# Kernel optimization log

Hardware: AMD Instinct MI355X
Metric: run time of the kernel (lower is better)

Reference implementation:

```python
import jax, jax.numpy as jnp
import numpy as np

N = 100000      # nodes
E = 1600000     # edges (before self loops)
IN_F = 128
OUT_F = 32
HEADS = 4
NEG_SLOPE = 0.2


def setup_inputs() -> dict:
    key = jax.random.key(0)
    k1, k2, k3, k4, k5, k6 = jax.random.split(key, 6)
    x = jax.random.normal(k1, (N, IN_F), dtype=jnp.float32)
    edge_index = jax.random.randint(k2, (2, E), 0, N, dtype=jnp.int64)
    # PyG GATConv params: shared linear W [in, H*F], attention vectors att_src/att_dst [1,H,F], bias [H*F]
    glorot = (6.0 / (IN_F + HEADS * OUT_F)) ** 0.5
    W = jax.random.uniform(k3, (IN_F, HEADS * OUT_F), dtype=jnp.float32, minval=-glorot, maxval=glorot)
    ga = (6.0 / (1 + OUT_F)) ** 0.5
    att_src = jax.random.uniform(k4, (HEADS, OUT_F), dtype=jnp.float32, minval=-ga, maxval=ga)
    att_dst = jax.random.uniform(k5, (HEADS, OUT_F), dtype=jnp.float32, minval=-ga, maxval=ga)
    bias = jnp.zeros((HEADS * OUT_F,), dtype=jnp.float32)
    return {"x": x, "edge_index": edge_index, "W": W, "att_src": att_src, "att_dst": att_dst, "bias": bias}


def reference(x, edge_index, W, att_src, att_dst, bias):
    n = x.shape[0]
    # add self loops (PyG add_self_loops=True)
    loops = jnp.arange(n, dtype=edge_index.dtype)
    src = jnp.concatenate([edge_index[0], loops])  # [E+N] message source j
    dst = jnp.concatenate([edge_index[1], loops])  # [E+N] message target i

    h = (x @ W).reshape(n, HEADS, OUT_F)                 # [N,H,F]
    a_src = jnp.sum(h * att_src[None], axis=-1)          # [N,H]
    a_dst = jnp.sum(h * att_dst[None], axis=-1)          # [N,H]

    e = a_src[src] + a_dst[dst]                          # [E',H]
    e = jax.nn.leaky_relu(e, NEG_SLOPE)
    # per-destination softmax over incoming edges
    m = jax.ops.segment_max(e, dst, num_segments=n)      # [N,H]
    ex = jnp.exp(e - m[dst])
    s = jax.ops.segment_sum(ex, dst, num_segments=n)     # [N,H]
    alpha = ex / (s[dst] + 1e-16)                        # [E',H]

    msg = h[src] * alpha[:, :, None]                     # [E',H,F]
    out = jax.ops.segment_sum(msg, dst, num_segments=n)  # [N,H,F]
    return out.reshape(n, HEADS * OUT_F) + bias
```

## Files before the change

kernel.cpp:

```cpp
#include <hip/hip_runtime.h>


#define NEG_SLOPE 0.2f
#define NB_MAX 256
#define BSHIFT 9
#define CHUNK 4096
#define BCAP 12288
#define CAP 11264
#define SS_STRIDE 11520
#define LOG2E 1.4426950408889634f

typedef __attribute__((ext_vector_type(8))) short short8;
typedef __attribute__((ext_vector_type(4))) float f32x4;
typedef __attribute__((ext_vector_type(2))) float f32x2;

__device__ __forceinline__ unsigned int rne16(unsigned int u) {
  return (u + 0x7fffu + ((u >> 16) & 1u)) >> 16;
}
__device__ __forceinline__ unsigned int f2bf_pack(float a, float b) {
  return (rne16(__float_as_uint(b)) << 16) | (rne16(__float_as_uint(a)) & 0xffffu);
}

__global__ __launch_bounds__(256) void k_prep(
    const float* __restrict__ W, unsigned short* __restrict__ Wt,
    int* __restrict__ bcnt) {
  int tid = threadIdx.x;
  if (blockIdx.x == 64) { bcnt[tid] = 0; return; }
  int idx = blockIdx.x * 256 + tid;
  int k = idx >> 7, col = idx & 127;
  Wt[col * 128 + k] = (unsigned short)rne16(__float_as_uint(W[idx]));
}

__global__ __launch_bounds__(256) void k_binmm(
    const int* __restrict__ ei, int* __restrict__ bcnt,
    unsigned int* __restrict__ binned, int E, int Nn, int nb, int nbBin,
    const float* __restrict__ x, const unsigned short* __restrict__ Wt,
    unsigned int* __restrict__ hb,
    const float* __restrict__ attS, const float* __restrict__ attD,
    float* __restrict__ aS, float* __restrict__ aD) {
  __shared__ unsigned int buf[CHUNK];
  __shared__ unsigned char bkt[CHUNK];
  __shared__ int hist[NB_MAX];
  __shared__ int loc[NB_MAX];
  __shared__ int gbase[NB_MAX];
  int tid = threadIdx.x;

  if ((int)blockIdx.x < nbBin) {
    int e0 = blockIdx.x * CHUNK;
    int n = E - e0; if (n > CHUNK) n = CHUNK;

    hist[tid] = 0;
    __syncthreads();

    int dstv[CHUNK / 256];
    int srcv[CHUNK / 256];
    int rankv[CHUNK / 256];
#pragma unroll
    for (int j = 0; j < CHUNK / 256; ++j) {
      int idx = j * 256 + tid;
      dstv[j] = -1;
      if (idx < n) {
        int d = ei[E + e0 + idx];
        srcv[j] = ei[e0 + idx];
        dstv[j] = d;
        rankv[j] = atomicAdd(&hist[d >> BSHIFT], 1);
      }
    }
    __syncthreads();

    if (tid < 64) {
      int base = tid * 4;
      int v0 = hist[base], v1 = hist[base + 1], v2 = hist[base + 2], v3 = hist[base + 3];
      int s = v0 + v1 + v2 + v3;
      int inc = s;
#pragma unroll
      for (int d = 1; d < 64; d <<= 1) {
        int t = __shfl_up(inc, d, 64);
        if (tid >= d) inc += t;
      }
      int ex = inc - s;
      loc[base] = ex; loc[base + 1] = ex + v0;
      loc[base + 2] = ex + v0 + v1; loc[base + 3] = ex + v0 + v1 + v2;
    }
    __syncthreads();

#pragma unroll
    for (int j = 0; j < CHUNK / 256; ++j) {
      if (dstv[j] >= 0) {
        int b = dstv[j] >> BSHIFT;
        int slot = loc[b] + rankv[j];
        buf[slot] = (unsigned)srcv[j] | ((unsigned)(dstv[j] & 511) << 20);
        bkt[slot] = (unsigned char)b;
      }
    }
    for (int b = tid; b < nb; b += 256)
      if (hist[b] > 0) gbase[b] = atomicAdd(&bcnt[b], hist[b]);
    __syncthreads();

    for (int s = tid; s < n; s += 256) {
      int b = bkt[s];
      binned[(unsigned)b * BCAP + gbase[b] + (s - loc[b])] = buf[s];
    }
    return;
  }

  int gbid = blockIdx.x - nbBin;
  int w = tid >> 6, lane = tid & 63;
  int m = lane & 15, q = lane >> 4;
  int r0 = gbid * 64 + w * 16;
  int rowA = r0 + m; if (rowA >= Nn) rowA = Nn - 1;
  const float* xrow = x + (unsigned)rowA * 128u;

  f32x4 acc[8];
#pragma unroll
  for (int t = 0; t < 8; ++t) acc[t] = (f32x4){0.f, 0.f, 0.f, 0.f};

#pragma unroll
  for (int ks = 0; ks < 4; ++ks) {
    int k0 = ks * 32 + q * 8;
    float4 a0 = *(const float4*)(xrow + k0);
    float4 a1 = *(const float4*)(xrow + k0 + 4);
    unsigned au[4];
    au[0] = f2bf_pack(a0.x, a0.y);
    au[1] = f2bf_pack(a0.z, a0.w);
    au[2] = f2bf_pack(a1.x, a1.y);
    au[3] = f2bf_pack(a1.z, a1.w);
    short8 af = *(short8*)au;
#pragma unroll
    for (int t = 0; t < 8; ++t) {
      short8 bf = *(const short8*)(Wt + (unsigned)(t * 16 + m) * 128u + k0);
      acc[t] = __builtin_amdgcn_mfma_f32_16x16x32_bf16(af, bf, acc[t], 0, 0, 0);
    }
  }

  float sSa[4], sSb[4], sDa[4], sDb[4];
#pragma unroll
  for (int u = 0; u < 4; ++u) {
    sSa[u] = attS[u * 32 + m]; sSb[u] = attS[u * 32 + m + 16];
    sDa[u] = attD[u * 32 + m]; sDb[u] = attD[u * 32 + m + 16];
  }

#pragma unroll
  for (int r = 0; r < 4; ++r) {
    int rowo = r0 + q * 4 + r;
    bool ok = rowo < Nn;
    if (ok) {
#pragma unroll
      for (int u = 0; u < 4; ++u)
        hb[(unsigned)rowo * 64u + u * 16 + m] = f2bf_pack(acc[2 * u][r], acc[2 * u + 1][r]);
    }
#pragma unroll
    for (int u = 0; u < 4; ++u) {
      float pS = acc[2 * u][r] * sSa[u] + acc[2 * u + 1][r] * sSb[u];
      float pD = acc[2 * u][r] * sDa[u] + acc[2 * u + 1][r] * sDb[u];
#pragma unroll
      for (int d = 8; d >= 1; d >>= 1) {
        pS += __shfl_down(pS, d, 16);
        pD += __shfl_down(pD, d, 16);
      }
      if (ok && m == 0) {
        aS[(unsigned)rowo * 4u + u] = pS * LOG2E;
        aD[(unsigned)rowo * 4u + u] = pD * LOG2E;
      }
    }
  }
}

__global__ __launch_bounds__(512) void k_scatter2(
    const unsigned int* __restrict__ binned, const int* __restrict__ bcnt,
    int2* __restrict__ off2, int* __restrict__ ssrc, int Nn) {
  __shared__ int cnt[512];
  __shared__ int obuf[CAP];
  __shared__ int wsum[8];
  int b = blockIdx.x, tid = threadIdx.x;
  int node0 = b << BSHIFT;
  int nnodes = Nn - node0; if (nnodes > 512) nnodes = 512;
  int nE = bcnt[b];
  const unsigned* bp = binned + (unsigned)b * BCAP;

  cnt[tid] = 0;
  __syncthreads();
  for (int i = tid; i < nE; i += 512)
    atomicAdd(&cnt[(bp[i] >> 20) & 511u], 1);
  __syncthreads();

  int v = cnt[tid] + (tid < nnodes ? 1 : 0);
  int lane = tid & 63, w = tid >> 6;
  int inc = v;
#pragma unroll
  for (int d = 1; d < 64; d <<= 1) {
    int t = __shfl_up(inc, d, 64);
    if (lane >= d) inc += t;
  }
  if (lane == 63) wsum[w] = inc;
  __syncthreads();
  int wbase = 0;
  for (int ww = 0; ww < w; ++ww) wbase += wsum[ww];
  int ex = wbase + inc - v;
  __syncthreads();

  int csrBase = b * SS_STRIDE;
  if (tid < nnodes) {
    off2[node0 + tid] = make_int2(csrBase + ex, v);
    obuf[ex] = node0 + tid;
  }
  cnt[tid] = ex + 1;
  __syncthreads();

  for (int i = tid; i < nE; i += 512) {
    unsigned p = bp[i];
    int d = (p >> 20) & 511u;
    int pos = atomicAdd(&cnt[d], 1);
    if (pos < CAP) obuf[pos] = (int)(p & 0xFFFFFu);
  }
  __syncthreads();

  int tot = nE + nnodes;
  for (int i = tid; i < tot; i += 512) ssrc[csrBase + i] = obuf[i];
}

__global__ __launch_bounds__(256) void k_aggregate(
    const unsigned int* __restrict__ hb, const float* __restrict__ aS, const float* __restrict__ aD,
    const int2* __restrict__ off2, const int* __restrict__ ssrc,
    const float* __restrict__ bias, float* __restrict__ out, int Nn) {
  int wave = threadIdx.x >> 6;
  int lane = threadIdx.x & 63;
  int node = blockIdx.x * 4 + wave;
  if (node >= Nn) return;
  int un = __builtin_amdgcn_readfirstlane(node);
  unsigned hd = (unsigned)lane >> 4;
  float ad = aD[(unsigned)un * 4u + hd];
  int2 o = off2[un];
  int p0 = o.x;
  int deg = o.y;
  const int* sp = ssrc + p0;
  int nch = deg >> 2;
  f32x2 acc = {0.f, 0.f};
  float denA = 0.f, denB = 0.f;

  int s0 = 0, s1 = 0, s2 = 0, s3 = 0;
  unsigned v0 = 0, v1 = 0, v2 = 0, v3 = 0;
  float a0 = 0.f, a1 = 0.f, a2 = 0.f, a3 = 0.f;
  if (nch > 0) {
    s0 = sp[0]; s1 = sp[1]; s2 = sp[2]; s3 = sp[3];
    v0 = hb[(unsigned)s0 * 64u + lane]; v1 = hb[(unsigned)s1 * 64u + lane];
    v2 = hb[(unsigned)s2 * 64u + lane]; v3 = hb[(unsigned)s3 * 64u + lane];
    a0 = aS[(unsigned)s0 * 4u + hd]; a1 = aS[(unsigned)s1 * 4u + hd];
    a2 = aS[(unsigned)s2 * 4u + hd]; a3 = aS[(unsigned)s3 * 4u + hd];
    sp += 4;
  }
  for (int c = 0; c < nch; ++c) {
    int t0 = 0, t1 = 0, t2 = 0, t3 = 0;
    unsigned w0 = 0, w1 = 0, w2 = 0, w3 = 0;
    float b0 = 0.f, b1 = 0.f, b2 = 0.f, b3 = 0.f;
    if (c + 1 < nch) {
      t0 = sp[0]; t1 = sp[1]; t2 = sp[2]; t3 = sp[3];
      w0 = hb[(unsigned)t0 * 64u + lane]; w1 = hb[(unsigned)t1 * 64u + lane];
      w2 = hb[(unsigned)t2 * 64u + lane]; w3 = hb[(unsigned)t3 * 64u + lane];
      b0 = aS[(unsigned)t0 * 4u + hd]; b1 = aS[(unsigned)t1 * 4u + hd];
      b2 = aS[(unsigned)t2 * 4u + hd]; b3 = aS[(unsigned)t3 * 4u + hd];
      sp += 4;
    }
    float e0 = a0 + ad, e1 = a1 + ad, e2 = a2 + ad, e3 = a3 + ad;
    e0 = fmaxf(e0, NEG_SLOPE * e0); e1 = fmaxf(e1, NEG_SLOPE * e1);
    e2 = fmaxf(e2, NEG_SLOPE * e2); e3 = fmaxf(e3, NEG_SLOPE * e3);
    float x0 = exp2f(e0), x1 = exp2f(e1), x2 = exp2f(e2), x3 = exp2f(e3);
    denA += x0 + x1; denB += x2 + x3;
    f32x2 h0 = { __uint_as_float(v0 << 16), __uint_as_float(v0 & 0xffff0000u) };
    f32x2 h1 = { __uint_as_float(v1 << 16), __uint_as_float(v1 & 0xffff0000u) };
    f32x2 h2 = { __uint_as_float(v2 << 16), __uint_as_float(v2 & 0xffff0000u) };
    f32x2 h3 = { __uint_as_float(v3 << 16), __uint_as_float(v3 & 0xffff0000u) };
    acc = h0 * x0 + acc;
    acc = h1 * x1 + acc;
    acc = h2 * x2 + acc;
    acc = h3 * x3 + acc;
    s0 = t0; s1 = t1; s2 = t2; s3 = t3;
    v0 = w0; v1 = w1; v2 = w2; v3 = w3;
    a0 = b0; a1 = b1; a2 = b2; a3 = b3;
  }
  for (int p = nch << 2; p < deg; ++p) {
    int src = (ssrc + p0)[p];
    float e = aS[(unsigned)src * 4u + hd] + ad;
    e = fmaxf(e, NEG_SLOPE * e);
    float ex = exp2f(e);
    unsigned v = hb[(unsigned)src * 64u + lane];
    f32x2 hh = { __uint_as_float(v << 16), __uint_as_float(v & 0xffff0000u) };
    acc = hh * ex + acc;
    denA += ex;
  }
  float inv = 1.0f / (denA + denB + 1e-16f);
  unsigned col = hd * 32u + ((unsigned)lane & 15u);
  out[(unsigned)un * 128u + col] = acc.x * inv + bias[col];
  out[(unsigned)un * 128u + col + 16u] = acc.y * inv + bias[col + 16];
}

extern "C" void kernel_launch(void* const* d_in, const int* in_sizes, int n_in,
                              void* d_out, int out_size, void* d_ws, size_t ws_size,
                              hipStream_t stream) {
  const float* x    = (const float*)d_in[0];
  const int*   ei   = (const int*)d_in[1];
  const float* W    = (const float*)d_in[2];
  const float* attS = (const float*)d_in[3];
  const float* attD = (const float*)d_in[4];
  const float* bias = (const float*)d_in[5];
  float* out = (float*)d_out;

  const int Nn = in_sizes[0] / 128;
  const int E  = in_sizes[1] / 2;
  const int nb = (Nn + (1 << BSHIFT) - 1) >> BSHIFT;
  const int nbBin = (E + CHUNK - 1) / CHUNK;
  const int nGemm = (Nn + 63) / 64;

  char* ws = (char*)d_ws;
  size_t o = 0;
  auto take = [&](size_t bytes) { void* p = ws + o; o += (bytes + 255) & ~(size_t)255; return p; };
  int2* off2     = (int2*)take((size_t)(Nn + 1) * 8);
  int* ssrc      = (int*)take((size_t)NB_MAX * SS_STRIDE * 4);
  int* bcnt      = (int*)take((size_t)NB_MAX * 4);
  float* aS      = (float*)take((size_t)Nn * 4 * 4);
  float* aD      = (float*)take((size_t)Nn * 4 * 4);
  unsigned short* Wt = (unsigned short*)take((size_t)128 * 128 * 2);
  unsigned int* hb = (unsigned int*)take((size_t)Nn * 64 * 4);
  unsigned int* binned = (unsigned int*)take((size_t)NB_MAX * BCAP * 4);
  (void)ws_size; (void)o;

  k_prep<<<65, 256, 0, stream>>>(W, Wt, bcnt);
  k_binmm<<<nbBin + nGemm, 256, 0, stream>>>(ei, bcnt, binned, E, Nn, nb, nbBin,
                                             x, Wt, hb, attS, attD, aS, aD);
  k_scatter2<<<nb, 512, 0, stream>>>(binned, bcnt, off2, ssrc, Nn);
  k_aggregate<<<(Nn + 3) / 4, 256, 0, stream>>>(hb, aS, aD, off2, ssrc, bias, out, Nn);
}
```

Before: 233.4 us.

## Split GEMM tiles across bin and scatter kernels; vectorize scatter loads and stores

The x@W GEMM tiles are split so that two thirds run alongside edge binning and the remaining third run as extra blocks in the scatter kernel. Each of those 512-thread scatter-kernel blocks computes two 256-thread GEMM tiles. This is meant to fill idle compute units, since the scatter kernel launches only about 196 blocks. Separately, the scatter kernel now reads binned entries as uint4 and writes the CSR source list as int4 to cut memory instruction count. The extra GEMM blocks still allocate the scatter kernel's large shared-memory footprint, which could limit how many of them run at once.

Measured after the change: 240.7 us. 3.1% more time.

```diff
diff --git a/kernel.cpp b/kernel.cpp
--- a/kernel.cpp
+++ b/kernel.cpp
@@ -29,6 +29,73 @@
   int idx = blockIdx.x * 256 + tid;
   int k = idx >> 7, col = idx & 127;
   Wt[col * 128 + k] = (unsigned short)rne16(__float_as_uint(W[idx]));
+}
+
+__device__ __forceinline__ void gemm_tile(
+    int gbid, int tid, int Nn,
+    const float* __restrict__ x, const unsigned short* __restrict__ Wt,
+    unsigned int* __restrict__ hb,
+    const float* __restrict__ attS, const float* __restrict__ attD,
+    float* __restrict__ aS, float* __restrict__ aD) {
+  int w = tid >> 6, lane = tid & 63;
+  int m = lane & 15, q = lane >> 4;
+  int r0 = gbid * 64 + w * 16;
+  int rowA = r0 + m; if (rowA >= Nn) rowA = Nn - 1;
+  const float* xrow = x + (unsigned)rowA * 128u;
+
+  f32x4 acc[8];
+#pragma unroll
+  for (int t = 0; t < 8; ++t) acc[t] = (f32x4){0.f, 0.f, 0.f, 0.f};
+
+#pragma unroll
+  for (int ks = 0; ks < 4; ++ks) {
+    int k0 = ks * 32 + q * 8;
+    float4 a0 = *(const float4*)(xrow + k0);
+    float4 a1 = *(const float4*)(xrow + k0 + 4);
+    unsigned au[4];
+    au[0] = f2bf_pack(a0.x, a0.y);
+    au[1] = f2bf_pack(a0.z, a0.w);
+    au[2] = f2bf_pack(a1.x, a1.y);
+    au[3] = f2bf_pack(a1.z, a1.w);
+    short8 af = *(short8*)au;
+#pragma unroll
+    for (int t = 0; t < 8; ++t) {
+      short8 bf = *(const short8*)(Wt + (unsigned)(t * 16 + m) * 128u + k0);
+      acc[t] = __builtin_amdgcn_mfma_f32_16x16x32_bf16(af, bf, acc[t], 0, 0, 0);
+    }
+  }
+
+  float sSa[4], sSb[4], sDa[4], sDb[4];
+#pragma unroll
+  for (int u = 0; u < 4; ++u) {
+    sSa[u] = attS[u * 32 + m]; sSb[u] = attS[u * 32 + m + 16];
+    sDa[u] = attD[u * 32 + m]; sDb[u] = attD[u * 32 + m + 16];
+  }
+
+#pragma unroll
+  for (int r = 0; r < 4; ++r) {
+    int rowo = r0 + q * 4 + r;
+    bool ok = rowo < Nn;
+    if (ok) {
+#pragma unroll
+      for (int u = 0; u < 4; ++u)
+        hb[(unsigned)rowo * 64u + u * 16 + m] = f2bf_pack(acc[2 * u][r], acc[2 * u + 1][r]);
+    }
+#pragma unroll
+    for (int u = 0; u < 4; ++u) {
+      float pS = acc[2 * u][r] * sSa[u] + acc[2 * u + 1][r] * sSb[u];
+      float pD = acc[2 * u][r] * sDa[u] + acc[2 * u + 1][r] * sDb[u];
+#pragma unroll
+      for (int d = 8; d >= 1; d >>= 1) {
+        pS += __shfl_down(pS, d, 16);
+        pD += __shfl_down(pD, d, 16);
+      }
+      if (ok && m == 0) {
+        aS[(unsigned)rowo * 4u + u] = pS * LOG2E;
+        aD[(unsigned)rowo * 4u + u] = pD * LOG2E;
+      }
+    }
+  }
 }
 
 __global__ __launch_bounds__(256) void k_binmm(
@@ -45,134 +112,86 @@
   __shared__ int gbase[NB_MAX];
   int tid = threadIdx.x;
 
-  if ((int)blockIdx.x < nbBin) {
-    int e0 = blockIdx.x * CHUNK;
-    int n = E - e0; if (n > CHUNK) n = CHUNK;
-
-    hist[tid] = 0;
-    __syncthreads();
-
-    int dstv[CHUNK / 256];
-    int srcv[CHUNK / 256];
-    int rankv[CHUNK / 256];
-#pragma unroll
-    for (int j = 0; j < CHUNK / 256; ++j) {
-      int idx = j * 256 + tid;
-      dstv[j] = -1;
-      if (idx < n) {
-        int d = ei[E + e0 + idx];
-        srcv[j] = ei[e0 + idx];
-        dstv[j] = d;
-        rankv[j] = atomicAdd(&hist[d >> BSHIFT], 1);
-      }
-    }
-    __syncthreads();
-
-    if (tid < 64) {
-      int base = tid * 4;
-      int v0 = hist[base], v1 = hist[base + 1], v2 = hist[base + 2], v3 = hist[base + 3];
-      int s = v0 + v1 + v2 + v3;
-      int inc = s;
-#pragma unroll
-      for (int d = 1; d < 64; d <<= 1) {
-        int t = __shfl_up(inc, d, 64);
-        if (tid >= d) inc += t;
-      }
-      int ex = inc - s;
-      loc[base] = ex; loc[base + 1] = ex + v0;
-      loc[base + 2] = ex + v0 + v1; loc[base + 3] = ex + v0 + v1 + v2;
-    }
-    __syncthreads();
-
-#pragma unroll
-    for (int j = 0; j < CHUNK / 256; ++j) {
-      if (dstv[j] >= 0) {
-        int b = dstv[j] >> BSHIFT;
-        int slot = loc[b] + rankv[j];
-        buf[slot] = (unsigned)srcv[j] | ((unsigned)(dstv[j] & 511) << 20);
-        bkt[slot] = (unsigned char)b;
-      }
-    }
-    for (int b = tid; b < nb; b += 256)
-      if (hist[b] > 0) gbase[b] = atomicAdd(&bcnt[b], hist[b]);
-    __syncthreads();
-
-    for (int s = tid; s < n; s += 256) {
-      int b = bkt[s];
-      binned[(unsigned)b * BCAP + gbase[b] + (s - loc[b])] = buf[s];
-    }
+  if ((int)blockIdx.x >= nbBin) {
+    gemm_tile(blockIdx.x - nbBin, tid, Nn, x, Wt, hb, attS, attD, aS, aD);
     return;
   }
 
-  int gbid = blockIdx.x - nbBin;
-  int w = tid >> 6, lane = tid & 63;
-  int m = lane & 15, q = lane >> 4;
-  int r0 = gbid * 64 + w * 16;
-  int rowA = r0 + m; if (rowA >= Nn) rowA = Nn - 1;
-  const float* xrow = x + (unsigned)rowA * 128u;
-
-  f32x4 acc[8];
-#pragma unroll
-  for (int t = 0; t < 8; ++t) acc[t] = (f32x4){0.f, 0.f, 0.f, 0.f};
-
-#pragma unroll
-  for (int ks = 0; ks < 4; ++ks) {
-    int k0 = ks * 32 + q * 8;
-    float4 a0 = *(const float4*)(xrow + k0);
-    float4 a1 = *(const float4*)(xrow + k0 + 4);
-    unsigned au[4];
-    au[0] = f2bf_pack(a0.x, a0.y);
-    au[1] = f2bf_pack(a0.z, a0.w);
-    au[2] = f2bf_pack(a1.x, a1.y);
-    au[3] = f2bf_pack(a1.z, a1.w);
-    short8 af = *(short8*)au;
-#pragma unroll
-    for (int t = 0; t < 8; ++t) {
-      short8 bf = *(const short8*)(Wt + (unsigned)(t * 16 + m) * 128u + k0);
-      acc[t] = __builtin_amdgcn_mfma_f32_16x16x32_bf16(af, bf, acc[t], 0, 0, 0);
-    }
-  }
-
-  float sSa[4], sSb[4], sDa[4], sDb[4];
-#pragma unroll
-  for (int u = 0; u < 4; ++u) {
-    sSa[u] = attS[u * 32 + m]; sSb[u] = attS[u * 32 + m + 16];
-    sDa[u] = attD[u * 32 + m]; sDb[u] = attD[u * 32 + m + 16];
-  }
-
-#pragma unroll
-  for (int r = 0; r < 4; ++r) {
-    int rowo = r0 + q * 4 + r;
-    bool ok = rowo < Nn;
-    if (ok) {
-#pragma unroll
-      for (int u = 0; u < 4; ++u)
-        hb[(unsigned)rowo * 64u + u * 16 + m] = f2bf_pack(acc[2 * u][r], acc[2 * u + 1][r]);
-    }
-#pragma unroll
-    for (int u = 0; u < 4; ++u) {
-      float pS = acc[2 * u][r] * sSa[u] + acc[2 * u + 1][r] * sSb[u];
-      float pD = acc[2 * u][r] * sDa[u] + acc[2 * u + 1][r] * sDb[u];
-#pragma unroll
-      for (int d = 8; d >= 1; d >>= 1) {
-        pS += __shfl_down(pS, d, 16);
-        pD += __shfl_down(pD, d, 16);
-      }
-      if (ok && m == 0) {
-        aS[(unsigned)rowo * 4u + u] = pS * LOG2E;
-        aD[(unsigned)rowo * 4u + u] = pD * LOG2E;
-      }
-    }
-  }
-}
-
-__global__ __launch_bounds__(512) void k_scatter2(
+  int e0 = blockIdx.x * CHUNK;
+  int n = E - e0; if (n > CHUNK) n = CHUNK;
+
+  hist[tid] = 0;
+  __syncthreads();
+
+  int dstv[CHUNK / 256];
+  int srcv[CHUNK / 256];
+  int rankv[CHUNK / 256];
+#pragma unroll
+  for (int j = 0; j < CHUNK / 256; ++j) {
+    int idx = j * 256 + tid;
+    dstv[j] = -1;
+    if (idx < n) {
+      int d = ei[E + e0 + idx];
+      srcv[j] = ei[e0 + idx];
+      dstv[j] = d;
+      rankv[j] = atomicAdd(&hist[d >> BSHIFT], 1);
+    }
+  }
+  __syncthreads();
+
+  if (tid < 64) {
+    int base = tid * 4;
+    int v0 = hist[base], v1 = hist[base + 1], v2 = hist[base + 2], v3 = hist[base + 3];
+    int s = v0 + v1 + v2 + v3;
+    int inc = s;
+#pragma unroll
+    for (int d = 1; d < 64; d <<= 1) {
+      int t = __shfl_up(inc, d, 64);
+      if (tid >= d) inc += t;
+    }
+    int ex = inc - s;
+    loc[base] = ex; loc[base + 1] = ex + v0;
+    loc[base + 2] = ex + v0 + v1; loc[base + 3] = ex + v0 + v1 + v2;
+  }
+  __syncthreads();
+
+#pragma unroll
+  for (int j = 0; j < CHUNK / 256; ++j) {
+    if (dstv[j] >= 0) {
+      int b = dstv[j] >> BSHIFT;
+      int slot = loc[b] + rankv[j];
+      buf[slot] = (unsigned)srcv[j] | ((unsigned)(dstv[j] & 511) << 20);
+      bkt[slot] = (unsigned char)b;
+    }
+  }
+  for (int b = tid; b < nb; b += 256)
+    if (hist[b] > 0) gbase[b] = atomicAdd(&bcnt[b], hist[b]);
+  __syncthreads();
+
+  for (int s = tid; s < n; s += 256) {
+    int b = bkt[s];
+    binned[(unsigned)b * BCAP + gbase[b] + (s - loc[b])] = buf[s];
+  }
+}
+
+__global__ __launch_bounds__(512) void k_scatgemm(
     const unsigned int* __restrict__ binned, const int* __restrict__ bcnt,
-    int2* __restrict__ off2, int* __restrict__ ssrc, int Nn) {
+    int2* __restrict__ off2, int* __restrict__ ssrc, int Nn, int nb, int nGemmA,
+    const float* __restrict__ x, const unsigned short* __restrict__ Wt,
+    unsigned int* __restrict__ hb,
+    const float* __restrict__ attS, const float* __restrict__ attD,
+    float* __restrict__ aS, float* __restrict__ aD) {
   __shared__ int cnt[512];
   __shared__ int obuf[CAP];
   __shared__ int wsum[8];
   int b = blockIdx.x, tid = threadIdx.x;
+
+  if (b >= nb) {
+    gemm_tile(nGemmA + (b - nb) * 2 + (tid >> 8), tid & 255, Nn,
+              x, Wt, hb, attS, attD, aS, aD);
+    return;
+  }
+
   int node0 = b << BSHIFT;
   int nnodes = Nn - node0; if (nnodes > 512) nnodes = 512;
   int nE = bcnt[b];
@@ -180,7 +199,15 @@
 
   cnt[tid] = 0;
   __syncthreads();
-  for (int i = tid; i < nE; i += 512)
+  int nE4 = nE >> 2;
+  for (int i = tid; i < nE4; i += 512) {
+    uint4 p = *(const uint4*)(bp + 4 * i);
+    atomicAdd(&cnt[(p.x >> 20) & 511u], 1);
+    atomicAdd(&cnt[(p.y >> 20) & 511u], 1);
+    atomicAdd(&cnt[(p.z >> 20) & 511u], 1);
+    atomicAdd(&cnt[(p.w >> 20) & 511u], 1);
+  }
+  for (int i = (nE4 << 2) + tid; i < nE; i += 512)
     atomicAdd(&cnt[(bp[i] >> 20) & 511u], 1);
   __syncthreads();
 
@@ -207,7 +234,14 @@
   cnt[tid] = ex + 1;
   __syncthreads();
 
-  for (int i = tid; i < nE; i += 512) {
+  for (int i = tid; i < nE4; i += 512) {
+    uint4 p = *(const uint4*)(bp + 4 * i);
+    { int d = (p.x >> 20) & 511u; int pos = atomicAdd(&cnt[d], 1); if (pos < CAP) obuf[pos] = (int)(p.x & 0xFFFFFu); }
+    { int d = (p.y >> 20) & 511u; int pos = atomicAdd(&cnt[d], 1); if (pos < CAP) obuf[pos] = (int)(p.y & 0xFFFFFu); }
+    { int d = (p.z >> 20) & 511u; int pos = atomicAdd(&cnt[d], 1); if (pos < CAP) obuf[pos] = (int)(p.z & 0xFFFFFu); }
+    { int d = (p.w >> 20) & 511u; int pos = atomicAdd(&cnt[d], 1); if (pos < CAP) obuf[pos] = (int)(p.w & 0xFFFFFu); }
+  }
+  for (int i = (nE4 << 2) + tid; i < nE; i += 512) {
     unsigned p = bp[i];
     int d = (p >> 20) & 511u;
     int pos = atomicAdd(&cnt[d], 1);
@@ -216,7 +250,11 @@
   __syncthreads();
 
   int tot = nE + nnodes;
-  for (int i = tid; i < tot; i += 512) ssrc[csrBase + i] = obuf[i];
+  int tot4 = tot >> 2;
+  for (int i = tid; i < tot4; i += 512)
+    *(int4*)(ssrc + csrBase + 4 * i) = *(const int4*)(obuf + 4 * i);
+  for (int i = (tot4 << 2) + tid; i < tot; i += 512)
+    ssrc[csrBase + i] = obuf[i];
 }
 
 __global__ __launch_bounds__(256) void k_aggregate(
@@ -310,6 +348,9 @@
   const int nb = (Nn + (1 << BSHIFT) - 1) >> BSHIFT;
   const int nbBin = (E + CHUNK - 1) / CHUNK;
   const int nGemm = (Nn + 63) / 64;
+  const int nGemmA = (nGemm * 2) / 3;
+  const int nGemmB = nGemm - nGemmA;
+  const int nFill = (nGemmB + 1) / 2;
 
   char* ws = (char*)d_ws;
   size_t o = 0;
@@ -325,8 +366,9 @@
   (void)ws_size; (void)o;
 
   k_prep<<<65, 256, 0, stream>>>(W, Wt, bcnt);
-  k_binmm<<<nbBin + nGemm, 256, 0, stream>>>(ei, bcnt, binned, E, Nn, nb, nbBin,
-                                             x, Wt, hb, attS, attD, aS, aD);
-  k_scatter2<<<nb, 512, 0, stream>>>(binned, bcnt, off2, ssrc, Nn);
+  k_binmm<<<nbBin + nGemmA, 256, 0, stream>>>(ei, bcnt, binned, E, Nn, nb, nbBin,
+                                              x, Wt, hb, attS, attD, aS, aD);
+  k_scatgemm<<<nb + nFill, 512, 0, stream>>>(binned, bcnt, off2, ssrc, Nn, nb,
+                                             nGemmA, x, Wt, hb, attS, attD, aS, aD);
   k_aggregate<<<(Nn + 3) / 4, 256, 0, stream>>>(hb, aS, aD, off2, ssrc, bias, out, Nn);
 }
```
